# Performance work log

Measured on AMD Instinct MI355X. Metric: run time of the kernel, lower is better.

Reference implementation:

```python
import jax, jax.numpy as jnp
import numpy as np

B, S, C = 16, 4096, 512


def setup_inputs() -> dict:
    key = jax.random.key(0)
    k1, k2, k3 = jax.random.split(key, 3)
    tag_logits_batch = jax.random.normal(k1, (B, S, C), dtype=jnp.float32)
    # probabilistic targets: normalize uniform draws so rows sum to 1
    t = jax.random.uniform(k2, (B, S, C), dtype=jnp.float32)
    target = t / jnp.sum(t, axis=-1, keepdims=True)
    mask = jax.random.randint(k3, (B, S), 0, 2, dtype=jnp.int32)
    return {"tag_logits_batch": tag_logits_batch, "target": target, "mask": mask}


def reference(tag_logits_batch, target, mask):
    # Soft-label cross-entropy per token: -sum_y target_y * log_softmax(logits)_y
    logp = jax.nn.log_softmax(tag_logits_batch, axis=-1)        # [B,S,C]
    tok_loss = -jnp.sum(target * logp, axis=-1)                  # [B,S]
    m = (mask == 1).astype(tok_loss.dtype)                       # [B,S]
    cnt = jnp.sum(m, axis=1)                                     # [B]
    # mean over active tokens per batch element (reduction='mean')
    per_batch = jnp.sum(tok_loss * m, axis=1) / jnp.maximum(cnt, 1.0)
    # torch code skips batch rows with no active tokens, then means over the rest
    has = (cnt > 0).astype(per_batch.dtype)                      # [B]
    return jnp.sum(per_batch * has) / jnp.maximum(jnp.sum(has), 1.0)
```

## Files before the change

### kernel.cpp

```cpp
#include <hip/hip_runtime.h>
#include <hip/hip_bf16.h>

#define BB 16
#define SS 4096
#define CC 512
#define NTOK (BB * SS)
#define LOSS_BLOCKS 2048
#define BLOCKS_PER_BATCH (LOSS_BLOCKS / BB)
#define WPB (BLOCKS_PER_BATCH * 4)


__global__ __launch_bounds__(256) void compact_kernel(
    const int* __restrict__ mask,
    int*       __restrict__ idxbuf,
    int*       __restrict__ cursors) {
    const int t     = blockIdx.x * 256 + threadIdx.x;
    const int batch = blockIdx.x / 16;
    const int lane  = threadIdx.x & 63;
    const int wave  = threadIdx.x >> 6;

    const bool active = (mask[t] == 1);
    unsigned long long ball = __ballot(active);
    const int prefix = __popcll(ball & ((1ull << lane) - 1ull));
    const int wcount = __popcll(ball);

    __shared__ int wbase[4];
    __shared__ int blockbase;
    if (lane == 0) wbase[wave] = wcount;
    __syncthreads();
    if (threadIdx.x == 0) {
        int total = wbase[0] + wbase[1] + wbase[2] + wbase[3];
        blockbase = atomicAdd(&cursors[batch], total);
        int s = 0;
        for (int i = 0; i < 4; ++i) { int c = wbase[i]; wbase[i] = s; s += c; }
    }
    __syncthreads();
    if (active)
        idxbuf[batch * SS + blockbase + wbase[wave] + prefix] = t;
}

__global__ __launch_bounds__(256, 8) void loss_kernel(
    const float* __restrict__ logits,
    const float* __restrict__ target,
    const int*   __restrict__ idxbuf,
    const int*   __restrict__ cursors,
    float*       __restrict__ partial) {
    const int wave  = threadIdx.x >> 6;
    const int lane  = threadIdx.x & 63;
    const int batch = blockIdx.x >> 7;
    const int wib   = (blockIdx.x & (BLOCKS_PER_BATCH - 1)) * 4 + wave;
    const int cnt   = cursors[batch];
    const int* list = idxbuf + batch * SS;

    float dotAcc = 0.0f;
    float logAcc = 0.0f;

    int k = wib;
    bool have = (k < cnt);
    float4 x0, x1, t0, t1;
    if (have) {
        const int tok = list[k];
        const float4* xp = (const float4*)(logits + (size_t)tok * CC);
        const float4* tp = (const float4*)(target + (size_t)tok * CC);
        x0 = xp[lane]; x1 = xp[lane + 64];
        t0 = tp[lane]; t1 = tp[lane + 64];
    }
    while (have) {
        const int kn = k + WPB;
        const bool haveN = (kn < cnt);
        float4 nx0, nx1, nt0, nt1;
        if (haveN) {
            const int tokN = list[kn];
            const float4* xp = (const float4*)(logits + (size_t)tokN * CC);
            const float4* tp = (const float4*)(target + (size_t)tokN * CC);
            nx0 = xp[lane]; nx1 = xp[lane + 64];
            nt0 = tp[lane]; nt1 = tp[lane + 64];
        }
        float se = __expf(x0.x) + __expf(x0.y) + __expf(x0.z) + __expf(x0.w)
                 + __expf(x1.x) + __expf(x1.y) + __expf(x1.z) + __expf(x1.w);
        dotAcc += t0.x * x0.x + t0.y * x0.y + t0.z * x0.z + t0.w * x0.w
                + t1.x * x1.x + t1.y * x1.y + t1.z * x1.z + t1.w * x1.w;
        #pragma unroll
        for (int off = 32; off >= 1; off >>= 1)
            se += __shfl_xor(se, off, 64);
        logAcc += __logf(se);
        x0 = nx0; x1 = nx1; t0 = nt0; t1 = nt1;
        k = kn; have = haveN;
    }

    #pragma unroll
    for (int off = 32; off >= 1; off >>= 1)
        dotAcc += __shfl_xor(dotAcc, off, 64);

    __shared__ float ls[4];
    if (lane == 0) ls[wave] = logAcc - dotAcc;
    __syncthreads();
    if (threadIdx.x == 0)
        partial[blockIdx.x] = ls[0] + ls[1] + ls[2] + ls[3];
}

__global__ __launch_bounds__(1024) void finalize_kernel(
    const float* __restrict__ partial,
    const int*   __restrict__ cursors,
    float*       __restrict__ out) {
    const int wave = threadIdx.x >> 6;
    const int lane = threadIdx.x & 63;

    float s = partial[wave * BLOCKS_PER_BATCH + lane]
            + partial[wave * BLOCKS_PER_BATCH + 64 + lane];
    #pragma unroll
    for (int off = 32; off >= 1; off >>= 1)
        s += __shfl_xor(s, off, 64);

    __shared__ float pb[BB], has[BB];
    if (lane == 0) {
        float c = (float)cursors[wave];
        pb[wave]  = (c > 0.0f) ? s / c : 0.0f;
        has[wave] = (c > 0.0f) ? 1.0f : 0.0f;
    }
    __syncthreads();
    if (threadIdx.x == 0) {
        float acc = 0.0f, nb = 0.0f;
        for (int b = 0; b < BB; ++b) { acc += pb[b]; nb += has[b]; }
        out[0] = acc / fmaxf(nb, 1.0f);
    }
}

extern "C" void kernel_launch(void* const* d_in, const int* in_sizes, int n_in,
                              void* d_out, int out_size, void* d_ws, size_t ws_size,
                              hipStream_t stream) {
    const float* logits = (const float*)d_in[0];
    const float* target = (const float*)d_in[1];
    const int*   mask   = (const int*)d_in[2];
    float* out     = (float*)d_out;
    int*   cursors = (int*)d_ws;
    int*   idxbuf  = (int*)((char*)d_ws + 128);
    float* partial = (float*)((char*)d_ws + 128 + NTOK * 4);

    hipMemsetAsync(cursors, 0, 64, stream);
    compact_kernel<<<NTOK / 256, 256, 0, stream>>>(mask, idxbuf, cursors);
    loss_kernel<<<LOSS_BLOCKS, 256, 0, stream>>>(logits, target, idxbuf, cursors, partial);
    finalize_kernel<<<1, 1024, 0, stream>>>(partial, cursors, out);
}
```

Before: 255.7 us.

## Fuse mask compaction into loss kernel via per-wave bitmask of strided tokens

Removes the memset and separate compaction kernel. Each wave now reads its 8 strided mask entries directly, builds a bitmask, and iterates over the set bits to load active tokens. Per-block active counts are written alongside the partial sums, and finalize reduces them to get per-batch counts. This saves two launches and the index-buffer round trip. In exchange, work is no longer balanced across waves, since each wave's load depends on how many of its own slots are active.

New measurement: 251.4 us. No clear change (-1.7%).

```diff
diff --git a/kernel.cpp b/kernel.cpp
--- a/kernel.cpp
+++ b/kernel.cpp
@@ -1,78 +1,57 @@
 #include <hip/hip_runtime.h>
-#include <hip/hip_bf16.h>
 
 #define BB 16
 #define SS 4096
 #define CC 512
-#define NTOK (BB * SS)
 #define LOSS_BLOCKS 2048
 #define BLOCKS_PER_BATCH (LOSS_BLOCKS / BB)
 #define WPB (BLOCKS_PER_BATCH * 4)
+#define SLOTS (SS / WPB)
 
-
-__global__ __launch_bounds__(256) void compact_kernel(
-    const int* __restrict__ mask,
-    int*       __restrict__ idxbuf,
-    int*       __restrict__ cursors) {
-    const int t     = blockIdx.x * 256 + threadIdx.x;
-    const int batch = blockIdx.x / 16;
-    const int lane  = threadIdx.x & 63;
-    const int wave  = threadIdx.x >> 6;
-
-    const bool active = (mask[t] == 1);
-    unsigned long long ball = __ballot(active);
-    const int prefix = __popcll(ball & ((1ull << lane) - 1ull));
-    const int wcount = __popcll(ball);
-
-    __shared__ int wbase[4];
-    __shared__ int blockbase;
-    if (lane == 0) wbase[wave] = wcount;
-    __syncthreads();
-    if (threadIdx.x == 0) {
-        int total = wbase[0] + wbase[1] + wbase[2] + wbase[3];
-        blockbase = atomicAdd(&cursors[batch], total);
-        int s = 0;
-        for (int i = 0; i < 4; ++i) { int c = wbase[i]; wbase[i] = s; s += c; }
-    }
-    __syncthreads();
-    if (active)
-        idxbuf[batch * SS + blockbase + wbase[wave] + prefix] = t;
-}
 
 __global__ __launch_bounds__(256, 8) void loss_kernel(
     const float* __restrict__ logits,
     const float* __restrict__ target,
-    const int*   __restrict__ idxbuf,
-    const int*   __restrict__ cursors,
-    float*       __restrict__ partial) {
+    const int*   __restrict__ mask,
+    float*       __restrict__ partial,
+    int*         __restrict__ pcnt) {
     const int wave  = threadIdx.x >> 6;
     const int lane  = threadIdx.x & 63;
     const int batch = blockIdx.x >> 7;
-    const int wib   = (blockIdx.x & (BLOCKS_PER_BATCH - 1)) * 4 + wave;
-    const int cnt   = cursors[batch];
-    const int* list = idxbuf + batch * SS;
+    const int wib   = ((blockIdx.x & (BLOCKS_PER_BATCH - 1)) << 2) + wave;
+
+    const int* __restrict__ mrow = mask + batch * SS;
+    const size_t rowbase = (size_t)batch * SS;
+
+    unsigned mb = 0u;
+    #pragma unroll
+    for (int j = 0; j < SLOTS; ++j)
+        mb |= (mrow[wib + j * WPB] == 1) ? (1u << j) : 0u;
+    const int cntw = __popc(mb);
 
     float dotAcc = 0.0f;
     float logAcc = 0.0f;
 
-    int k = wib;
-    bool have = (k < cnt);
+    bool have = (mb != 0u);
+    unsigned rem = 0u;
     float4 x0, x1, t0, t1;
     if (have) {
-        const int tok = list[k];
-        const float4* xp = (const float4*)(logits + (size_t)tok * CC);
-        const float4* tp = (const float4*)(target + (size_t)tok * CC);
+        const int j = __ffs(mb) - 1;
+        rem = mb & (mb - 1u);
+        const size_t tok = rowbase + (size_t)(wib + j * WPB);
+        const float4* xp = (const float4*)(logits + tok * CC);
+        const float4* tp = (const float4*)(target + tok * CC);
         x0 = xp[lane]; x1 = xp[lane + 64];
         t0 = tp[lane]; t1 = tp[lane + 64];
     }
     while (have) {
-        const int kn = k + WPB;
-        const bool haveN = (kn < cnt);
+        const bool haveN = (rem != 0u);
         float4 nx0, nx1, nt0, nt1;
         if (haveN) {
-            const int tokN = list[kn];
-            const float4* xp = (const float4*)(logits + (size_t)tokN * CC);
-            const float4* tp = (const float4*)(target + (size_t)tokN * CC);
+            const int jn = __ffs(rem) - 1;
+            const size_t tokN = rowbase + (size_t)(wib + jn * WPB);
+            const float4* xp = (const float4*)(logits + tokN * CC);
+            const float4* tp = (const float4*)(target + tokN * CC);
             nx0 = xp[lane]; nx1 = xp[lane + 64];
             nt0 = tp[lane]; nt1 = tp[lane + 64];
         }
@@ -85,7 +64,7 @@
             se += __shfl_xor(se, off, 64);
         logAcc += __logf(se);
         x0 = nx0; x1 = nx1; t0 = nt0; t1 = nt1;
-        k = kn; have = haveN;
+        rem &= (rem - 1u); have = haveN;
     }
 
     #pragma unroll
@@ -93,28 +72,34 @@
         dotAcc += __shfl_xor(dotAcc, off, 64);
 
     __shared__ float ls[4];
-    if (lane == 0) ls[wave] = logAcc - dotAcc;
+    __shared__ int   lc[4];
+    if (lane == 0) { ls[wave] = logAcc - dotAcc; lc[wave] = cntw; }
     __syncthreads();
-    if (threadIdx.x == 0)
+    if (threadIdx.x == 0) {
         partial[blockIdx.x] = ls[0] + ls[1] + ls[2] + ls[3];
+        pcnt[blockIdx.x]    = lc[0] + lc[1] + lc[2] + lc[3];
+    }
 }
 
 __global__ __launch_bounds__(1024) void finalize_kernel(
     const float* __restrict__ partial,
-    const int*   __restrict__ cursors,
+    const int*   __restrict__ pcnt,
     float*       __restrict__ out) {
     const int wave = threadIdx.x >> 6;
     const int lane = threadIdx.x & 63;
 
     float s = partial[wave * BLOCKS_PER_BATCH + lane]
             + partial[wave * BLOCKS_PER_BATCH + 64 + lane];
+    float c = (float)(pcnt[wave * BLOCKS_PER_BATCH + lane]
+                    + pcnt[wave * BLOCKS_PER_BATCH + 64 + lane]);
     #pragma unroll
-    for (int off = 32; off >= 1; off >>= 1)
+    for (int off = 32; off >= 1; off >>= 1) {
         s += __shfl_xor(s, off, 64);
+        c += __shfl_xor(c, off, 64);
+    }
 
     __shared__ float pb[BB], has[BB];
     if (lane == 0) {
-        float c = (float)cursors[wave];
         pb[wave]  = (c > 0.0f) ? s / c : 0.0f;
         has[wave] = (c > 0.0f) ? 1.0f : 0.0f;
     }
@@ -133,12 +118,9 @@
     const float* target = (const float*)d_in[1];
     const int*   mask   = (const int*)d_in[2];
     float* out     = (float*)d_out;
-    int*   cursors = (int*)d_ws;
-    int*   idxbuf  = (int*)((char*)d_ws + 128);
-    float* partial = (float*)((char*)d_ws + 128 + NTOK * 4);
+    float* partial = (float*)d_ws;
+    int*   pcnt    = (int*)((char*)d_ws + 8192);
 
-    hipMemsetAsync(cursors, 0, 64, stream);
-    compact_kernel<<<NTOK / 256, 256, 0, stream>>>(mask, idxbuf, cursors);
-    loss_kernel<<<LOSS_BLOCKS, 256, 0, stream>>>(logits, target, idxbuf, cursors, partial);
-    finalize_kernel<<<1, 1024, 0, stream>>>(partial, cursors, out);
+    loss_kernel<<<LOSS_BLOCKS, 256, 0, stream>>>(logits, target, mask, partial, pcnt);
+    finalize_kernel<<<1, 1024, 0, stream>>>(partial, pcnt, out);
 }
```
